# Kernel optimization log

Hardware: AMD Instinct MI355X
Metric: run time of the kernel (lower is better)

## Reference

```python
import jax, jax.numpy as jnp
import numpy as np

D_MODEL = 1024
H = 16
DK = 64
DV = 64
D_OUT = 1024
SEQ = 1024
BATCH = 4


def setup_inputs() -> dict:
    key = jax.random.key(0)
    ks = jax.random.split(key, 11)
    s = 0.02
    return {
        "query": jax.random.normal(ks[0], (SEQ, BATCH, D_MODEL), jnp.float32),
        "key": jax.random.normal(ks[1], (SEQ, BATCH, D_MODEL), jnp.float32),
        "value": jax.random.normal(ks[2], (SEQ, BATCH, D_MODEL), jnp.float32),
        "Wq": jax.random.normal(ks[3], (D_MODEL, H * DK), jnp.float32) * s,
        "bq": jnp.zeros((H * DK,), jnp.float32),
        "Wk": jax.random.normal(ks[4], (D_MODEL, H * DK), jnp.float32) * s,
        "bk": jnp.zeros((H * DK,), jnp.float32),
        "Wv": jax.random.normal(ks[5], (D_MODEL, H * DV), jnp.float32) * s,
        "bv": jnp.zeros((H * DV,), jnp.float32),
        "Wo": jax.random.normal(ks[6], (H * DV, D_OUT), jnp.float32) * s,
        "bo": jnp.zeros((D_OUT,), jnp.float32),
    }


def reference(query, key, value, Wq, bq, Wk, bk, Wv, bv, Wo, bo):
    S, B, _ = query.shape
    # projections (seq-first layout, like the torch module)
    q = query @ Wq + bq            # (S, B, H*DK)
    k = key @ Wk + bk              # (S, B, H*DK)
    v = value @ Wv + bv            # (S, B, H*DV)
    # view + transpose(0, 2): (S, B, H, d) -> (H, B, S, d)
    q = jnp.transpose(q.reshape(S, B, H, DK), (2, 1, 0, 3))
    k = jnp.transpose(k.reshape(S, B, H, DK), (2, 1, 0, 3))
    v = jnp.transpose(v.reshape(S, B, H, DV), (2, 1, 0, 3))
    # scaled dot-product attention, full logits materialized as in the original
    logits = jnp.einsum("hbsd,hbtd->hbst", q, k) / jnp.sqrt(jnp.float32(DK))
    attn = jax.nn.softmax(logits, axis=-1)            # (H, B, S, S)
    ctx = jnp.einsum("hbst,hbtd->hbsd", attn, v)       # (H, B, S, DV)
    # transpose(0, 2) back and merge heads: (S, B, H*DV)
    ctx = jnp.transpose(ctx, (2, 1, 0, 3)).reshape(S, B, H * DV)
    out = ctx @ Wo + bo                               # (S, B, D_OUT)
    return (out, attn)
```

## Files before the change

### kernel.cpp

```cpp
#include <hip/hip_runtime.h>


typedef unsigned short u16;
typedef unsigned int u32;
typedef short short8v __attribute__((ext_vector_type(8)));
typedef float f32x4 __attribute__((ext_vector_type(4)));

__device__ __forceinline__ u16 f2bf(float f) {
    u32 u = __builtin_bit_cast(u32, f);
    u += 0x7fffu + ((u >> 16) & 1u);
    return (u16)(u >> 16);
}

__device__ __forceinline__ f32x4 mfma_bf16(short8v a, short8v b, f32x4 c) {
    return __builtin_amdgcn_mfma_f32_16x16x32_bf16(a, b, c, 0, 0, 0);
}

__global__ __launch_bounds__(256) void cvt_transpose_w(const float* __restrict__ W,
                                                       u16* __restrict__ Wt) {
    __shared__ u16 T[64][72];
    const int n0 = (blockIdx.x & 15) << 6;
    const int k0 = (blockIdx.x >> 4) << 6;
    const int t = threadIdx.x;
    const int r = t >> 2;
    const int c = t & 3;
    const float4* src = reinterpret_cast<const float4*>(W + (size_t)(k0 + r) * 1024 + n0 + c * 16);
#pragma unroll
    for (int j = 0; j < 4; ++j) {
        float4 v = src[j];
        T[c * 16 + j * 4 + 0][r] = f2bf(v.x);
        T[c * 16 + j * 4 + 1][r] = f2bf(v.y);
        T[c * 16 + j * 4 + 2][r] = f2bf(v.z);
        T[c * 16 + j * 4 + 3][r] = f2bf(v.w);
    }
    __syncthreads();
    u16* dst = Wt + (size_t)(n0 + r) * 1024 + k0 + c * 16;
    *reinterpret_cast<short8v*>(dst)     = *reinterpret_cast<const short8v*>(&T[r][c * 16]);
    *reinterpret_cast<short8v*>(dst + 8) = *reinterpret_cast<const short8v*>(&T[r][c * 16 + 8]);
}

template <int AMODE, int EMODE>
__global__ __launch_bounds__(256) void gemm_kernel(const void* __restrict__ A_,
                                                   const u16* __restrict__ Wt,
                                                   const float* __restrict__ bias,
                                                   void* __restrict__ dst_) {
    __shared__ u16 As[128][40];
    __shared__ u16 Bs[128][40];
    const int m0 = blockIdx.y << 7;
    const int n0 = blockIdx.x << 7;
    const int t = threadIdx.x;
    const int lane = t & 63;
    const int w = t >> 6;
    const int wr = (w >> 1) << 6;
    const int wc = (w & 1) << 6;
    const int l15 = lane & 15, lg = lane >> 4;
    const int srow = t >> 1;
    const int shalf = (t & 1) << 4;

    f32x4 acc[4][4] = {};

    for (int k0 = 0; k0 < 1024; k0 += 32) {
        if (AMODE == 0) {
            const float* A = (const float*)A_;
            const float4* src = reinterpret_cast<const float4*>(A + (size_t)(m0 + srow) * 1024 + k0 + shalf);
            float4 v0 = src[0], v1 = src[1], v2 = src[2], v3 = src[3];
            short8v p0, p1;
            p0[0] = f2bf(v0.x); p0[1] = f2bf(v0.y); p0[2] = f2bf(v0.z); p0[3] = f2bf(v0.w);
            p0[4] = f2bf(v1.x); p0[5] = f2bf(v1.y); p0[6] = f2bf(v1.z); p0[7] = f2bf(v1.w);
            p1[0] = f2bf(v2.x); p1[1] = f2bf(v2.y); p1[2] = f2bf(v2.z); p1[3] = f2bf(v2.w);
            p1[4] = f2bf(v3.x); p1[5] = f2bf(v3.y); p1[6] = f2bf(v3.z); p1[7] = f2bf(v3.w);
            *reinterpret_cast<short8v*>(&As[srow][shalf])     = p0;
            *reinterpret_cast<short8v*>(&As[srow][shalf + 8]) = p1;
        } else {
            const u16* A = (const u16*)A_;
            const short8v* src = reinterpret_cast<const short8v*>(A + (size_t)(m0 + srow) * 1024 + k0 + shalf);
            *reinterpret_cast<short8v*>(&As[srow][shalf])     = src[0];
            *reinterpret_cast<short8v*>(&As[srow][shalf + 8]) = src[1];
        }
        {
            const short8v* src = reinterpret_cast<const short8v*>(Wt + (size_t)(n0 + srow) * 1024 + k0 + shalf);
            *reinterpret_cast<short8v*>(&Bs[srow][shalf])     = src[0];
            *reinterpret_cast<short8v*>(&Bs[srow][shalf + 8]) = src[1];
        }
        __syncthreads();
        short8v a[4], b[4];
#pragma unroll
        for (int m = 0; m < 4; ++m)
            a[m] = *reinterpret_cast<const short8v*>(&As[wr + m * 16 + l15][lg * 8]);
#pragma unroll
        for (int n = 0; n < 4; ++n)
            b[n] = *reinterpret_cast<const short8v*>(&Bs[wc + n * 16 + l15][lg * 8]);
#pragma unroll
        for (int m = 0; m < 4; ++m)
#pragma unroll
            for (int n = 0; n < 4; ++n)
                acc[m][n] = mfma_bf16(a[m], b[n], acc[m][n]);
        __syncthreads();
    }

#pragma unroll
    for (int n = 0; n < 4; ++n) {
        const int c = n0 + wc + n * 16 + l15;
        const float bv = bias[c];
#pragma unroll
        for (int m = 0; m < 4; ++m) {
#pragma unroll
            for (int r = 0; r < 4; ++r) {
                const int mi = m0 + wr + m * 16 + lg * 4 + r;
                const float val = acc[m][n][r] + bv;
                if (EMODE == 0) {
                    u16* dst = (u16*)dst_;
                    const int h = c >> 6, d = c & 63, s = mi >> 2, bb = mi & 3;
                    dst[(size_t)(((h << 2) + bb) << 16) + (s << 6) + d] = f2bf(val);
                } else {
                    float* dst = (float*)dst_;
                    dst[(size_t)mi * 1024 + c] = val;
                }
            }
        }
    }
}

__global__ __launch_bounds__(256) void transpose_v(const u16* __restrict__ vb,
                                                   u16* __restrict__ vtb) {
    __shared__ u16 T[64][72];
    const int hb = blockIdx.y;
    const int s0 = blockIdx.x << 6;
    const u16* src = vb + (size_t)hb * 65536;
    u16* dst = vtb + (size_t)hb * 65536;
    const int t = threadIdx.x;
    const int r = t >> 2;
    const int c = (t & 3) << 4;
    short8v v0 = *reinterpret_cast<const short8v*>(src + (size_t)(s0 + r) * 64 + c);
    short8v v1 = *reinterpret_cast<const short8v*>(src + (size_t)(s0 + r) * 64 + c + 8);
#pragma unroll
    for (int j = 0; j < 8; ++j) T[c + j][r] = (u16)v0[j];
#pragma unroll
    for (int j = 0; j < 8; ++j) T[c + 8 + j][r] = (u16)v1[j];
    __syncthreads();
    *reinterpret_cast<short8v*>(dst + (size_t)r * 1024 + s0 + c)     = *reinterpret_cast<const short8v*>(&T[r][c]);
    *reinterpret_cast<short8v*>(dst + (size_t)r * 1024 + s0 + c + 8) = *reinterpret_cast<const short8v*>(&T[r][c + 8]);
}

__global__ __launch_bounds__(512, 1) void attn_kernel(const u16* __restrict__ qb,
                                                      const u16* __restrict__ kb,
                                                      const u16* __restrict__ vtb,
                                                      float* __restrict__ attn_out,
                                                      u16* __restrict__ ctxb) {
    __shared__ float S[32 * 1024];
    const int hb = blockIdx.y;
    const int q0 = blockIdx.x << 5;
    const int h = hb >> 2, b = hb & 3;
    const int t = threadIdx.x;
    const int lane = t & 63, w = t >> 6;
    const int l15 = lane & 15, lg = lane >> 4;

    const u16* Q = qb + (size_t)hb * 65536;
    const u16* K = kb + (size_t)hb * 65536;
    const u16* VT = vtb + (size_t)hb * 65536;

    short8v aq[2][2];
#pragma unroll
    for (int m = 0; m < 2; ++m)
#pragma unroll
        for (int kh = 0; kh < 2; ++kh)
            aq[m][kh] = *reinterpret_cast<const short8v*>(Q + (q0 + m * 16 + l15) * 64 + kh * 32 + lg * 8);

#pragma unroll
    for (int n = 0; n < 8; ++n) {
        const int tcol = w * 128 + n * 16 + l15;
        f32x4 s0acc = {}, s1acc = {};
#pragma unroll
        for (int kh = 0; kh < 2; ++kh) {
            short8v bk = *reinterpret_cast<const short8v*>(K + tcol * 64 + kh * 32 + lg * 8);
            s0acc = mfma_bf16(aq[0][kh], bk, s0acc);
            s1acc = mfma_bf16(aq[1][kh], bk, s1acc);
        }
#pragma unroll
        for (int r = 0; r < 4; ++r) {
            const int row0 = lg * 4 + r;
            const int row1 = 16 + row0;
            S[row0 * 1024 + ((tcol + row0 * 8) & 1023)] = s0acc[r] * 0.125f;
            S[row1 * 1024 + ((tcol + row1 * 8) & 1023)] = s1acc[r] * 0.125f;
        }
    }
    __syncthreads();

#pragma unroll
    for (int rr = 0; rr < 4; ++rr) {
        const int r = w * 4 + rr;
        const int rot = r * 8;
        float v[16];
        float mx = -1e30f;
#pragma unroll
        for (int j = 0; j < 16; ++j) {
            v[j] = S[r * 1024 + ((j * 64 + lane + rot) & 1023)];
            mx = fmaxf(mx, v[j]);
        }
#pragma unroll
        for (int o = 1; o < 64; o <<= 1) mx = fmaxf(mx, __shfl_xor(mx, o, 64));
        float sum = 0.f;
#pragma unroll
        for (int j = 0; j < 16; ++j) { v[j] = __expf(v[j] - mx); sum += v[j]; }
#pragma unroll
        for (int o = 1; o < 64; o <<= 1) sum += __shfl_xor(sum, o, 64);
        const float inv = 1.0f / sum;
        float* grow = attn_out + (size_t)(hb * 1024 + q0 + r) * 1024;
#pragma unroll
        for (int j = 0; j < 16; ++j) {
            const float p = v[j] * inv;
            S[r * 1024 + ((j * 64 + lane + rot) & 1023)] = p;
            grow[j * 64 + lane] = p;
        }
    }
    __syncthreads();

    f32x4 cacc[2][4] = {};
#pragma unroll
    for (int kt = 0; kt < 4; ++kt) {
        short8v ap[2];
#pragma unroll
        for (int m = 0; m < 2; ++m) {
            const int row = m * 16 + l15;
            const int col = (w * 128 + kt * 32 + lg * 8 + row * 8) & 1023;
            const f32x4 lo = *reinterpret_cast<const f32x4*>(&S[row * 1024 + col]);
            const f32x4 hi = *reinterpret_cast<const f32x4*>(&S[row * 1024 + col + 4]);
            short8v p;
#pragma unroll
            for (int j = 0; j < 4; ++j) { p[j] = (short)f2bf(lo[j]); p[4 + j] = (short)f2bf(hi[j]); }
            ap[m] = p;
        }
#pragma unroll
        for (int n = 0; n < 4; ++n) {
            short8v bv = *reinterpret_cast<const short8v*>(VT + (size_t)(n * 16 + l15) * 1024 + w * 128 + kt * 32 + lg * 8);
            cacc[0][n] = mfma_bf16(ap[0], bv, cacc[0][n]);
            cacc[1][n] = mfma_bf16(ap[1], bv, cacc[1][n]);
        }
    }
    __syncthreads();
    float* part = S;
#pragma unroll
    for (int m = 0; m < 2; ++m)
#pragma unroll
        for (int n = 0; n < 4; ++n)
#pragma unroll
            for (int r = 0; r < 4; ++r)
                part[(w * 32 + m * 16 + lg * 4 + r) * 64 + n * 16 + l15] = cacc[m][n][r];
    __syncthreads();
    {
        const int e = t * 4;
        const int rrow = e >> 6, col = e & 63;
        f32x4 sum4 = {};
#pragma unroll
        for (int ww = 0; ww < 8; ++ww)
            sum4 += *reinterpret_cast<const f32x4*>(&part[(ww * 32 + rrow) * 64 + col]);
        u16* dst = ctxb + (size_t)((q0 + rrow) * 4 + b) * 1024 + h * 64 + col;
        dst[0] = f2bf(sum4[0]); dst[1] = f2bf(sum4[1]); dst[2] = f2bf(sum4[2]); dst[3] = f2bf(sum4[3]);
    }
}

extern "C" void kernel_launch(void* const* d_in, const int* in_sizes, int n_in,
                              void* d_out, int out_size, void* d_ws, size_t ws_size,
                              hipStream_t stream) {
    const float* query = (const float*)d_in[0];
    const float* key   = (const float*)d_in[1];
    const float* value = (const float*)d_in[2];
    const float* Wq = (const float*)d_in[3];
    const float* bq = (const float*)d_in[4];
    const float* Wk = (const float*)d_in[5];
    const float* bk = (const float*)d_in[6];
    const float* Wv = (const float*)d_in[7];
    const float* bv = (const float*)d_in[8];
    const float* Wo = (const float*)d_in[9];
    const float* bo = (const float*)d_in[10];

    char* ws = (char*)d_ws;
    u16* Wtq  = (u16*)(ws);
    u16* Wtk  = (u16*)(ws + ((size_t)2 << 20));
    u16* Wtv  = (u16*)(ws + ((size_t)4 << 20));
    u16* Wto  = (u16*)(ws + ((size_t)6 << 20));
    u16* qb   = (u16*)(ws + ((size_t)8 << 20));
    u16* kb   = (u16*)(ws + ((size_t)16 << 20));
    u16* vb   = (u16*)(ws + ((size_t)24 << 20));
    u16* vtb  = (u16*)(ws + ((size_t)32 << 20));
    u16* ctxb = (u16*)(ws + ((size_t)24 << 20));

    float* out  = (float*)d_out;
    float* attn = out + (size_t)4 * 1024 * 1024;

    cvt_transpose_w<<<256, 256, 0, stream>>>(Wq, Wtq);
    cvt_transpose_w<<<256, 256, 0, stream>>>(Wk, Wtk);
    cvt_transpose_w<<<256, 256, 0, stream>>>(Wv, Wtv);
    cvt_transpose_w<<<256, 256, 0, stream>>>(Wo, Wto);

    gemm_kernel<0, 0><<<dim3(8, 32), 256, 0, stream>>>(query, Wtq, bq, qb);
    gemm_kernel<0, 0><<<dim3(8, 32), 256, 0, stream>>>(key,   Wtk, bk, kb);
    gemm_kernel<0, 0><<<dim3(8, 32), 256, 0, stream>>>(value, Wtv, bv, vb);

    transpose_v<<<dim3(16, 64), 256, 0, stream>>>(vb, vtb);

    attn_kernel<<<dim3(32, 64), 512, 0, stream>>>(qb, kb, vtb, attn, ctxb);

    gemm_kernel<1, 1><<<dim3(8, 32), 256, 0, stream>>>(ctxb, Wto, bo, out);
}
```

Measured before the change: 597.6 us.

## Batch weight/QKV launches, prefetch GEMM tiles, shrink attention tile, split-K output GEMM

Merges the four weight conversions into one launch and the three QKV projections into one grid. The projection GEMM now uses a 64-wide K tile with register prefetch of the next tile. The attention kernel takes 16 query rows per block instead of 32, stores bf16 probabilities in an XOR-swizzled LDS layout and writes the attn output with vector stores, so more blocks fit per CU. The output projection becomes a 512-thread split-K kernel that reduces its two halves through LDS. The aim is to cut launch overhead, hide global load latency and raise occupancy, at the cost of more LDS per block and an extra reduction step.

```diff
diff --git a/kernel.cpp b/kernel.cpp
--- a/kernel.cpp
+++ b/kernel.cpp
@@ -4,6 +4,7 @@
 typedef unsigned short u16;
 typedef unsigned int u32;
 typedef short short8v __attribute__((ext_vector_type(8)));
+typedef short short4v __attribute__((ext_vector_type(4)));
 typedef float f32x4 __attribute__((ext_vector_type(4)));
 
 __device__ __forceinline__ u16 f2bf(float f) {
@@ -16,9 +17,20 @@
     return __builtin_amdgcn_mfma_f32_16x16x32_bf16(a, b, c, 0, 0, 0);
 }
 
-__global__ __launch_bounds__(256) void cvt_transpose_w(const float* __restrict__ W,
-                                                       u16* __restrict__ Wt) {
+__global__ __launch_bounds__(256) void cvt_transpose_w4(const float* __restrict__ W0,
+                                                        const float* __restrict__ W1,
+                                                        const float* __restrict__ W2,
+                                                        const float* __restrict__ W3,
+                                                        u16* __restrict__ T0, u16* __restrict__ T1,
+                                                        u16* __restrict__ T2, u16* __restrict__ T3) {
     __shared__ u16 T[64][72];
+    const float* W; u16* Wt;
+    switch (blockIdx.y) {
+        case 0: W = W0; Wt = T0; break;
+        case 1: W = W1; Wt = T1; break;
+        case 2: W = W2; Wt = T2; break;
+        default: W = W3; Wt = T3; break;
+    }
     const int n0 = (blockIdx.x & 15) << 6;
     const int k0 = (blockIdx.x >> 4) << 6;
     const int t = threadIdx.x;
@@ -39,13 +51,25 @@
     *reinterpret_cast<short8v*>(dst + 8) = *reinterpret_cast<const short8v*>(&T[r][c * 16 + 8]);
 }
 
-template <int AMODE, int EMODE>
-__global__ __launch_bounds__(256) void gemm_kernel(const void* __restrict__ A_,
-                                                   const u16* __restrict__ Wt,
-                                                   const float* __restrict__ bias,
-                                                   void* __restrict__ dst_) {
-    __shared__ u16 As[128][40];
-    __shared__ u16 Bs[128][40];
+__global__ __launch_bounds__(256, 2) void gemm_qkv(const float* __restrict__ Aq,
+                                                   const float* __restrict__ Ak,
+                                                   const float* __restrict__ Av,
+                                                   const u16* __restrict__ Wtq,
+                                                   const u16* __restrict__ Wtk,
+                                                   const u16* __restrict__ Wtv,
+                                                   const float* __restrict__ bq,
+                                                   const float* __restrict__ bk,
+                                                   const float* __restrict__ bv,
+                                                   u16* __restrict__ dq, u16* __restrict__ dk,
+                                                   u16* __restrict__ dv) {
+    __shared__ u16 As[128][72];
+    __shared__ u16 Bs[128][72];
+    const float* A; const u16* Wt; const float* bias; u16* dst;
+    switch (blockIdx.z) {
+        case 0: A = Aq; Wt = Wtq; bias = bq; dst = dq; break;
+        case 1: A = Ak; Wt = Wtk; bias = bk; dst = dk; break;
+        default: A = Av; Wt = Wtv; bias = bv; dst = dv; break;
+    }
     const int m0 = blockIdx.y << 7;
     const int n0 = blockIdx.x << 7;
     const int t = threadIdx.x;
@@ -55,67 +79,68 @@
     const int wc = (w & 1) << 6;
     const int l15 = lane & 15, lg = lane >> 4;
     const int srow = t >> 1;
-    const int shalf = (t & 1) << 4;
+    const int sh = (t & 1) << 5;
+
+    const float* Arow = A + (size_t)(m0 + srow) * 1024 + sh;
+    const u16*   Brow = Wt + (size_t)(n0 + srow) * 1024 + sh;
 
     f32x4 acc[4][4] = {};
-
-    for (int k0 = 0; k0 < 1024; k0 += 32) {
-        if (AMODE == 0) {
-            const float* A = (const float*)A_;
-            const float4* src = reinterpret_cast<const float4*>(A + (size_t)(m0 + srow) * 1024 + k0 + shalf);
-            float4 v0 = src[0], v1 = src[1], v2 = src[2], v3 = src[3];
-            short8v p0, p1;
-            p0[0] = f2bf(v0.x); p0[1] = f2bf(v0.y); p0[2] = f2bf(v0.z); p0[3] = f2bf(v0.w);
-            p0[4] = f2bf(v1.x); p0[5] = f2bf(v1.y); p0[6] = f2bf(v1.z); p0[7] = f2bf(v1.w);
-            p1[0] = f2bf(v2.x); p1[1] = f2bf(v2.y); p1[2] = f2bf(v2.z); p1[3] = f2bf(v2.w);
-            p1[4] = f2bf(v3.x); p1[5] = f2bf(v3.y); p1[6] = f2bf(v3.z); p1[7] = f2bf(v3.w);
-            *reinterpret_cast<short8v*>(&As[srow][shalf])     = p0;
-            *reinterpret_cast<short8v*>(&As[srow][shalf + 8]) = p1;
-        } else {
-            const u16* A = (const u16*)A_;
-            const short8v* src = reinterpret_cast<const short8v*>(A + (size_t)(m0 + srow) * 1024 + k0 + shalf);
-            *reinterpret_cast<short8v*>(&As[srow][shalf])     = src[0];
-            *reinterpret_cast<short8v*>(&As[srow][shalf + 8]) = src[1];
-        }
-        {
-            const short8v* src = reinterpret_cast<const short8v*>(Wt + (size_t)(n0 + srow) * 1024 + k0 + shalf);
-            *reinterpret_cast<short8v*>(&Bs[srow][shalf])     = src[0];
-            *reinterpret_cast<short8v*>(&Bs[srow][shalf + 8]) = src[1];
-        }
+    float4 ra[8]; short8v rb[4];
+
+    auto LOADR = [&](int kt) {
+        const float4* ap = reinterpret_cast<const float4*>(Arow + kt * 64);
+#pragma unroll
+        for (int j = 0; j < 8; ++j) ra[j] = ap[j];
+        const short8v* bp = reinterpret_cast<const short8v*>(Brow + kt * 64);
+#pragma unroll
+        for (int j = 0; j < 4; ++j) rb[j] = bp[j];
+    };
+
+    LOADR(0);
+    for (int kt = 0; kt < 16; ++kt) {
         __syncthreads();
-        short8v a[4], b[4];
-#pragma unroll
-        for (int m = 0; m < 4; ++m)
-            a[m] = *reinterpret_cast<const short8v*>(&As[wr + m * 16 + l15][lg * 8]);
-#pragma unroll
-        for (int n = 0; n < 4; ++n)
-            b[n] = *reinterpret_cast<const short8v*>(&Bs[wc + n * 16 + l15][lg * 8]);
-#pragma unroll
-        for (int m = 0; m < 4; ++m)
+#pragma unroll
+        for (int j = 0; j < 4; ++j) {
+            float4 x = ra[2 * j], y = ra[2 * j + 1];
+            short8v p;
+            p[0] = (short)f2bf(x.x); p[1] = (short)f2bf(x.y);
+            p[2] = (short)f2bf(x.z); p[3] = (short)f2bf(x.w);
+            p[4] = (short)f2bf(y.x); p[5] = (short)f2bf(y.y);
+            p[6] = (short)f2bf(y.z); p[7] = (short)f2bf(y.w);
+            *reinterpret_cast<short8v*>(&As[srow][sh + j * 8]) = p;
+            *reinterpret_cast<short8v*>(&Bs[srow][sh + j * 8]) = rb[j];
+        }
+        if (kt < 15) LOADR(kt + 1);
+        __syncthreads();
+#pragma unroll
+        for (int kk = 0; kk < 2; ++kk) {
+            short8v a[4], b[4];
+#pragma unroll
+            for (int m = 0; m < 4; ++m)
+                a[m] = *reinterpret_cast<const short8v*>(&As[wr + m * 16 + l15][kk * 32 + lg * 8]);
 #pragma unroll
             for (int n = 0; n < 4; ++n)
-                acc[m][n] = mfma_bf16(a[m], b[n], acc[m][n]);
-        __syncthreads();
+                b[n] = *reinterpret_cast<const short8v*>(&Bs[wc + n * 16 + l15][kk * 32 + lg * 8]);
+#pragma unroll
+            for (int m = 0; m < 4; ++m)
+#pragma unroll
+                for (int n = 0; n < 4; ++n)
+                    acc[m][n] = mfma_bf16(a[m], b[n], acc[m][n]);
+        }
     }
 
 #pragma unroll
     for (int n = 0; n < 4; ++n) {
         const int c = n0 + wc + n * 16 + l15;
-        const float bv = bias[c];
+        const float bvv = bias[c];
+        const int h = c >> 6, d = c & 63;
 #pragma unroll
         for (int m = 0; m < 4; ++m) {
 #pragma unroll
             for (int r = 0; r < 4; ++r) {
                 const int mi = m0 + wr + m * 16 + lg * 4 + r;
-                const float val = acc[m][n][r] + bv;
-                if (EMODE == 0) {
-                    u16* dst = (u16*)dst_;
-                    const int h = c >> 6, d = c & 63, s = mi >> 2, bb = mi & 3;
-                    dst[(size_t)(((h << 2) + bb) << 16) + (s << 6) + d] = f2bf(val);
-                } else {
-                    float* dst = (float*)dst_;
-                    dst[(size_t)mi * 1024 + c] = val;
-                }
+                const int s = mi >> 2, bb = mi & 3;
+                dst[(size_t)(((h << 2) + bb) << 16) + (s << 6) + d] = f2bf(acc[m][n][r] + bvv);
             }
         }
     }
@@ -142,14 +167,15 @@
     *reinterpret_cast<short8v*>(dst + (size_t)r * 1024 + s0 + c + 8) = *reinterpret_cast<const short8v*>(&T[r][c + 8]);
 }
 
-__global__ __launch_bounds__(512, 1) void attn_kernel(const u16* __restrict__ qb,
+__global__ __launch_bounds__(512, 4) void attn_kernel(const u16* __restrict__ qb,
                                                       const u16* __restrict__ kb,
                                                       const u16* __restrict__ vtb,
                                                       float* __restrict__ attn_out,
                                                       u16* __restrict__ ctxb) {
-    __shared__ float S[32 * 1024];
+    __shared__ float Sm[16 * 1024];
+    char* Sb = (char*)Sm;
     const int hb = blockIdx.y;
-    const int q0 = blockIdx.x << 5;
+    const int q0 = blockIdx.x << 4;
     const int h = hb >> 2, b = hb & 3;
     const int t = threadIdx.x;
     const int lane = t & 63, w = t >> 6;
@@ -159,103 +185,187 @@
     const u16* K = kb + (size_t)hb * 65536;
     const u16* VT = vtb + (size_t)hb * 65536;
 
-    short8v aq[2][2];
-#pragma unroll
-    for (int m = 0; m < 2; ++m)
-#pragma unroll
-        for (int kh = 0; kh < 2; ++kh)
-            aq[m][kh] = *reinterpret_cast<const short8v*>(Q + (q0 + m * 16 + l15) * 64 + kh * 32 + lg * 8);
+    short8v aq[2];
+#pragma unroll
+    for (int kh = 0; kh < 2; ++kh)
+        aq[kh] = *reinterpret_cast<const short8v*>(Q + (q0 + l15) * 64 + kh * 32 + lg * 8);
 
 #pragma unroll
     for (int n = 0; n < 8; ++n) {
         const int tcol = w * 128 + n * 16 + l15;
-        f32x4 s0acc = {}, s1acc = {};
+        f32x4 acc = {};
 #pragma unroll
         for (int kh = 0; kh < 2; ++kh) {
             short8v bk = *reinterpret_cast<const short8v*>(K + tcol * 64 + kh * 32 + lg * 8);
-            s0acc = mfma_bf16(aq[0][kh], bk, s0acc);
-            s1acc = mfma_bf16(aq[1][kh], bk, s1acc);
+            acc = mfma_bf16(aq[kh], bk, acc);
         }
 #pragma unroll
         for (int r = 0; r < 4; ++r) {
-            const int row0 = lg * 4 + r;
-            const int row1 = 16 + row0;
-            S[row0 * 1024 + ((tcol + row0 * 8) & 1023)] = s0acc[r] * 0.125f;
-            S[row1 * 1024 + ((tcol + row1 * 8) & 1023)] = s1acc[r] * 0.125f;
-        }
-    }
-    __syncthreads();
-
-#pragma unroll
-    for (int rr = 0; rr < 4; ++rr) {
-        const int r = w * 4 + rr;
-        const int rot = r * 8;
-        float v[16];
+            const int row = lg * 4 + r;
+            *(float*)(Sb + (row << 12) + (((tcol) << 2) ^ ((row & 7) << 4))) = acc[r] * 0.125f;
+        }
+    }
+    __syncthreads();
+
+#pragma unroll
+    for (int rr = 0; rr < 2; ++rr) {
+        const int r = w * 2 + rr;
+        const int swz = (r & 7) << 4;
+        f32x4 vv[4];
+#pragma unroll
+        for (int j = 0; j < 4; ++j)
+            vv[j] = *(const f32x4*)(Sb + (r << 12) + (((lane * 4 + j * 256) << 2) ^ swz));
         float mx = -1e30f;
 #pragma unroll
-        for (int j = 0; j < 16; ++j) {
-            v[j] = S[r * 1024 + ((j * 64 + lane + rot) & 1023)];
-            mx = fmaxf(mx, v[j]);
-        }
+        for (int j = 0; j < 4; ++j)
+#pragma unroll
+            for (int i = 0; i < 4; ++i) mx = fmaxf(mx, vv[j][i]);
 #pragma unroll
         for (int o = 1; o < 64; o <<= 1) mx = fmaxf(mx, __shfl_xor(mx, o, 64));
         float sum = 0.f;
 #pragma unroll
-        for (int j = 0; j < 16; ++j) { v[j] = __expf(v[j] - mx); sum += v[j]; }
+        for (int j = 0; j < 4; ++j)
+#pragma unroll
+            for (int i = 0; i < 4; ++i) { vv[j][i] = __expf(vv[j][i] - mx); sum += vv[j][i]; }
 #pragma unroll
         for (int o = 1; o < 64; o <<= 1) sum += __shfl_xor(sum, o, 64);
         const float inv = 1.0f / sum;
-        float* grow = attn_out + (size_t)(hb * 1024 + q0 + r) * 1024;
-#pragma unroll
-        for (int j = 0; j < 16; ++j) {
-            const float p = v[j] * inv;
-            S[r * 1024 + ((j * 64 + lane + rot) & 1023)] = p;
-            grow[j * 64 + lane] = p;
-        }
-    }
-    __syncthreads();
-
-    f32x4 cacc[2][4] = {};
+        float* grow = attn_out + (((size_t)(hb << 10) + q0 + r) << 10);
+#pragma unroll
+        for (int j = 0; j < 4; ++j) {
+            f32x4 p = vv[j] * inv;
+            *reinterpret_cast<f32x4*>(grow + lane * 4 + j * 256) = p;
+            short4v pk;
+            pk[0] = (short)f2bf(p[0]); pk[1] = (short)f2bf(p[1]);
+            pk[2] = (short)f2bf(p[2]); pk[3] = (short)f2bf(p[3]);
+            *(short4v*)(Sb + (r << 12) + (((lane * 4 + j * 256) << 1) ^ swz)) = pk;
+        }
+    }
+    __syncthreads();
+
+    f32x4 cacc[4] = {};
 #pragma unroll
     for (int kt = 0; kt < 4; ++kt) {
-        short8v ap[2];
-#pragma unroll
-        for (int m = 0; m < 2; ++m) {
-            const int row = m * 16 + l15;
-            const int col = (w * 128 + kt * 32 + lg * 8 + row * 8) & 1023;
-            const f32x4 lo = *reinterpret_cast<const f32x4*>(&S[row * 1024 + col]);
-            const f32x4 hi = *reinterpret_cast<const f32x4*>(&S[row * 1024 + col + 4]);
-            short8v p;
-#pragma unroll
-            for (int j = 0; j < 4; ++j) { p[j] = (short)f2bf(lo[j]); p[4 + j] = (short)f2bf(hi[j]); }
-            ap[m] = p;
-        }
+        const int kcol = w * 128 + kt * 32 + lg * 8;
+        short8v ap = *(const short8v*)(Sb + (l15 << 12) + (((kcol) << 1) ^ ((l15 & 7) << 4)));
 #pragma unroll
         for (int n = 0; n < 4; ++n) {
-            short8v bv = *reinterpret_cast<const short8v*>(VT + (size_t)(n * 16 + l15) * 1024 + w * 128 + kt * 32 + lg * 8);
-            cacc[0][n] = mfma_bf16(ap[0], bv, cacc[0][n]);
-            cacc[1][n] = mfma_bf16(ap[1], bv, cacc[1][n]);
-        }
-    }
-    __syncthreads();
-    float* part = S;
-#pragma unroll
-    for (int m = 0; m < 2; ++m)
-#pragma unroll
-        for (int n = 0; n < 4; ++n)
-#pragma unroll
-            for (int r = 0; r < 4; ++r)
-                part[(w * 32 + m * 16 + lg * 4 + r) * 64 + n * 16 + l15] = cacc[m][n][r];
-    __syncthreads();
-    {
-        const int e = t * 4;
-        const int rrow = e >> 6, col = e & 63;
-        f32x4 sum4 = {};
+            short8v bv = *reinterpret_cast<const short8v*>(VT + (size_t)(n * 16 + l15) * 1024 + kcol);
+            cacc[n] = mfma_bf16(ap, bv, cacc[n]);
+        }
+    }
+    __syncthreads();
+
+    float* part = Sm;
+#pragma unroll
+    for (int n = 0; n < 4; ++n)
+#pragma unroll
+        for (int r = 0; r < 4; ++r)
+            part[w * 1088 + (lg * 4 + r) * 68 + n * 16 + l15] = cacc[n][r];
+    __syncthreads();
+    if (t < 256) {
+        const int rrow = t >> 4;
+        const int c0 = (t & 15) << 2;
+        f32x4 s = {};
 #pragma unroll
         for (int ww = 0; ww < 8; ++ww)
-            sum4 += *reinterpret_cast<const f32x4*>(&part[(ww * 32 + rrow) * 64 + col]);
-        u16* dst = ctxb + (size_t)((q0 + rrow) * 4 + b) * 1024 + h * 64 + col;
-        dst[0] = f2bf(sum4[0]); dst[1] = f2bf(sum4[1]); dst[2] = f2bf(sum4[2]); dst[3] = f2bf(sum4[3]);
+            s += *reinterpret_cast<const f32x4*>(&part[ww * 1088 + rrow * 68 + c0]);
+        short4v o;
+        o[0] = (short)f2bf(s[0]); o[1] = (short)f2bf(s[1]);
+        o[2] = (short)f2bf(s[2]); o[3] = (short)f2bf(s[3]);
+        *reinterpret_cast<short4v*>(ctxb + (size_t)(((q0 + rrow) << 2) + b) * 1024 + h * 64 + c0) = o;
+    }
+}
+
+__global__ __launch_bounds__(512, 2) void gemm_out(const u16* __restrict__ ctxb,
+                                                   const u16* __restrict__ Wto,
+                                                   const float* __restrict__ bo,
+                                                   float* __restrict__ out) {
+    __shared__ char LB[73728];
+    const int m0 = blockIdx.y << 7;
+    const int n0 = blockIdx.x << 7;
+    const int t = threadIdx.x;
+    const int lane = t & 63;
+    const int w = t >> 6;
+    const int grp = w >> 2;
+    const int wl = w & 3;
+    const int wr = (wl >> 1) << 6;
+    const int wc = (wl & 1) << 6;
+    const int l15 = lane & 15, lg = lane >> 4;
+    const int tg = t & 255;
+    const int srow = tg >> 1;
+    const int sh = (tg & 1) << 5;
+
+    u16 (*As)[72] = (u16(*)[72])(LB + grp * 36864);
+    u16 (*Bs)[72] = (u16(*)[72])(LB + grp * 36864 + 18432);
+    const int kb0 = grp << 9;
+
+    const u16* Arow = ctxb + (size_t)(m0 + srow) * 1024 + kb0 + sh;
+    const u16* Brow = Wto + (size_t)(n0 + srow) * 1024 + kb0 + sh;
+
+    f32x4 acc[4][4] = {};
+    short8v ra[4], rb[4];
+
+    auto LOADR = [&](int s) {
+        const short8v* ap = reinterpret_cast<const short8v*>(Arow + s * 64);
+        const short8v* bp = reinterpret_cast<const short8v*>(Brow + s * 64);
+#pragma unroll
+        for (int j = 0; j < 4; ++j) { ra[j] = ap[j]; rb[j] = bp[j]; }
+    };
+
+    LOADR(0);
+    for (int s = 0; s < 8; ++s) {
+        __syncthreads();
+#pragma unroll
+        for (int j = 0; j < 4; ++j) {
+            *reinterpret_cast<short8v*>(&As[srow][sh + j * 8]) = ra[j];
+            *reinterpret_cast<short8v*>(&Bs[srow][sh + j * 8]) = rb[j];
+        }
+        if (s < 7) LOADR(s + 1);
+        __syncthreads();
+#pragma unroll
+        for (int kk = 0; kk < 2; ++kk) {
+            short8v a[4], b[4];
+#pragma unroll
+            for (int m = 0; m < 4; ++m)
+                a[m] = *reinterpret_cast<const short8v*>(&As[wr + m * 16 + l15][kk * 32 + lg * 8]);
+#pragma unroll
+            for (int n = 0; n < 4; ++n)
+                b[n] = *reinterpret_cast<const short8v*>(&Bs[wc + n * 16 + l15][kk * 32 + lg * 8]);
+#pragma unroll
+            for (int m = 0; m < 4; ++m)
+#pragma unroll
+                for (int n = 0; n < 4; ++n)
+                    acc[m][n] = mfma_bf16(a[m], b[n], acc[m][n]);
+        }
+    }
+
+    __syncthreads();
+    float* part = (float*)LB;
+    if (grp == 1) {
+#pragma unroll
+        for (int m = 0; m < 4; ++m)
+#pragma unroll
+            for (int n = 0; n < 4; ++n)
+#pragma unroll
+                for (int r = 0; r < 4; ++r)
+                    part[(wr + m * 16 + lg * 4 + r) * 132 + wc + n * 16 + l15] = acc[m][n][r];
+    }
+    __syncthreads();
+    if (grp == 0) {
+#pragma unroll
+        for (int n = 0; n < 4; ++n) {
+            const int c = n0 + wc + n * 16 + l15;
+            const float bvv = bo[c];
+#pragma unroll
+            for (int m = 0; m < 4; ++m)
+#pragma unroll
+                for (int r = 0; r < 4; ++r) {
+                    const int mi = m0 + wr + m * 16 + lg * 4 + r;
+                    out[(size_t)mi * 1024 + c] =
+                        acc[m][n][r] + part[(wr + m * 16 + lg * 4 + r) * 132 + wc + n * 16 + l15] + bvv;
+                }
+        }
     }
 }
 
@@ -288,18 +398,14 @@
     float* out  = (float*)d_out;
     float* attn = out + (size_t)4 * 1024 * 1024;
 
-    cvt_transpose_w<<<256, 256, 0, stream>>>(Wq, Wtq);
-    cvt_transpose_w<<<256, 256, 0, stream>>>(Wk, Wtk);
-    cvt_transpose_w<<<256, 256, 0, stream>>>(Wv, Wtv);
-    cvt_transpose_w<<<256, 256, 0, stream>>>(Wo, Wto);
-
-    gemm_kernel<0, 0><<<dim3(8, 32), 256, 0, stream>>>(query, Wtq, bq, qb);
-    gemm_kernel<0, 0><<<dim3(8, 32), 256, 0, stream>>>(key,   Wtk, bk, kb);
-    gemm_kernel<0, 0><<<dim3(8, 32), 256, 0, stream>>>(value, Wtv, bv, vb);
+    cvt_transpose_w4<<<dim3(256, 4), 256, 0, stream>>>(Wq, Wk, Wv, Wo, Wtq, Wtk, Wtv, Wto);
+
+    gemm_qkv<<<dim3(8, 32, 3), 256, 0, stream>>>(query, key, value, Wtq, Wtk, Wtv,
+                                                 bq, bk, bv, qb, kb, vb);
 
     transpose_v<<<dim3(16, 64), 256, 0, stream>>>(vb, vtb);
 
-    attn_kernel<<<dim3(32, 64), 512, 0, stream>>>(qb, kb, vtb, attn, ctxb);
-
-    gemm_kernel<1, 1><<<dim3(8, 32), 256, 0, stream>>>(ctxb, Wto, bo, out);
-}
+    attn_kernel<<<dim3(64, 64), 512, 0, stream>>>(qb, kb, vtb, attn, ctxb);
+
+    gemm_out<<<dim3(8, 32), 512, 0, stream>>>(ctxb, Wto, bo, out);
+}
```

Measured after the change: 529.6 us. 11.4% less time.
